# Kernel optimization log

Measured on AMD Instinct MI355X. Metric: run time of the kernel, lower is better.

Reference implementation:

```python
import jax, jax.numpy as jnp
import numpy as np

T, B, OBS, H, A = 512, 256, 128, 256, 32

def setup_inputs() -> dict:
    key = jax.random.key(0)
    ks = jax.random.split(key, 16)
    s = 0.05
    return {
        'hidden': jnp.zeros((B, H), jnp.float32),
        'obs': jax.random.normal(ks[0], (T, B, OBS), jnp.float32),
        'dones': jax.random.bernoulli(ks[1], 0.1, (T, B)),
        'avail_actions': (jax.random.uniform(ks[2], (T, B, A)) > 0.1).astype(jnp.float32),
        'W_emb': jax.random.normal(ks[3], (OBS, H), jnp.float32) * s,
        'b_emb': jnp.zeros((H,), jnp.float32),
        'Wi': jax.random.normal(ks[4], (H, 3 * H), jnp.float32) * s,
        'bi': jnp.zeros((3 * H,), jnp.float32),
        'Whr': jax.random.normal(ks[5], (H, H), jnp.float32) * s,
        'Whz': jax.random.normal(ks[6], (H, H), jnp.float32) * s,
        'Whn': jax.random.normal(ks[7], (H, H), jnp.float32) * s,
        'bhn': jnp.zeros((H,), jnp.float32),
        'W_a1': jax.random.normal(ks[8], (H, H), jnp.float32) * s,
        'b_a1': jnp.zeros((H,), jnp.float32),
        'W_a2': jax.random.normal(ks[9], (H, A), jnp.float32) * s,
        'b_a2': jnp.zeros((A,), jnp.float32),
        'W_c1': jax.random.normal(ks[10], (H, H), jnp.float32) * s,
        'b_c1': jnp.zeros((H,), jnp.float32),
        'W_c2': jax.random.normal(ks[11], (H, 1), jnp.float32) * s,
        'b_c2': jnp.zeros((1,), jnp.float32),
    }

def reference(hidden, obs, dones, avail_actions, W_emb, b_emb, Wi, bi,
              Whr, Whz, Whn, bhn, W_a1, b_a1, W_a2, b_a2, W_c1, b_c1, W_c2, b_c2):
    # obs embedding + relu: [T,B,OBS] -> [T,B,H]
    emb = jax.nn.relu(obs @ W_emb + b_emb)
    # precompute input gate projections for all timesteps (same math as per-step Dense)
    gi = emb @ Wi + bi  # [T,B,3H]

    def step(h, xs):
        gi_t, done_t = xs
        h = jnp.where(done_t[:, None], 0.0, h)  # reset-select to zero init carry
        ir, iz, inn = jnp.split(gi_t, 3, axis=-1)
        r = jax.nn.sigmoid(ir + h @ Whr)
        z = jax.nn.sigmoid(iz + h @ Whz)
        n = jnp.tanh(inn + r * (h @ Whn + bhn))
        h_new = (1.0 - z) * n + z * h
        return h_new, h_new

    hidden_out, y = jax.lax.scan(step, hidden, (gi, dones))  # y: [T,B,H]

    actor_h = jax.nn.relu(y @ W_a1 + b_a1)
    actor_mean = actor_h @ W_a2 + b_a2  # [T,B,A]
    logits = actor_mean - (1.0 - avail_actions) * 1e10

    critic_h = jax.nn.relu(y @ W_c1 + b_c1)
    value = jnp.squeeze(critic_h @ W_c2 + b_c2, axis=-1)  # [T,B]
    return hidden_out, logits, value
```

## Files before the change

### kernel.cpp

```cpp
#include <hip/hip_runtime.h>
#include <stdint.h>

#define T_DIM 512
#define B_DIM 256
#define OBS_DIM 128
#define H_DIM 256
#define A_DIM 32
#define TB (T_DIM*B_DIM)

typedef unsigned short u16;
typedef unsigned int   u32;
typedef _Float16 half2v __attribute__((ext_vector_type(2)));
typedef __attribute__((ext_vector_type(8))) short short8;
typedef __attribute__((ext_vector_type(4))) float f32x4;
typedef __attribute__((ext_vector_type(4))) u32   u32x4;

__device__ __forceinline__ float bf2f(u16 v){ return __uint_as_float(((u32)v)<<16); }
__device__ __forceinline__ u16 f2bf(float f){
    u32 x = __float_as_uint(f);
    u32 r = x + 0x7fffu + ((x>>16)&1u);
    return (u16)(r>>16);
}
__device__ __forceinline__ float2 bfpair(u32 u){
    return make_float2(__uint_as_float(u<<16), __uint_as_float(u & 0xffff0000u));
}

__device__ __forceinline__ float dot2(u32 a, u32 b, float c){
#if __has_builtin(__builtin_amdgcn_fdot2)
    return __builtin_amdgcn_fdot2(__builtin_bit_cast(half2v,a),
                                  __builtin_bit_cast(half2v,b), c, false);
#else
    half2v ha = __builtin_bit_cast(half2v,a), hb = __builtin_bit_cast(half2v,b);
    return fmaf((float)ha[0],(float)hb[0], fmaf((float)ha[1],(float)hb[1], c));
#endif
}

#define DOT2A(acc, w, h) \
    asm("v_dot2_f32_f16 %0, %1, %2, %0" : "+v"(acc) : "v"(w), "v"(h))

#define GLOAD16(gsrc, ldst) \
    __builtin_amdgcn_global_load_lds( \
        (const __attribute__((address_space(1))) void*)(gsrc), \
        (__attribute__((address_space(3))) void*)(ldst), 16, 0, 0)

__global__ void zero_flags_kernel(int* p){ if(threadIdx.x<4) p[threadIdx.x]=0; }

__global__ void detect_kernel(const unsigned char* __restrict__ d, int n, int* __restrict__ flags){
    int f=0;
    for(int p = blockIdx.x*blockDim.x+threadIdx.x; p<n; p += gridDim.x*blockDim.x){
        if(d[p]){ int m=p&3; if(m==1) f|=1; else if(m>=2) f|=2; }
    }
    if(f) atomicOr(flags, f);
}

__global__ void concat_bias_kernel(const float* __restrict__ a, const float* __restrict__ b,
                                   float* __restrict__ dst){
    int i = threadIdx.x;
    dst[i] = a[i];
    dst[256 + i] = b[i];
}

__global__ void cvt_wt_kernel(const float* __restrict__ Whr, const float* __restrict__ Whz,
                              const float* __restrict__ Whn, u32* __restrict__ dst){
    int i = blockIdx.x*blockDim.x + threadIdx.x;
    if(i >= 3*32*256*4) return;
    int e = i & 3;
    int j = (i >> 2) & 255;
    int q = (i >> 10) & 31;
    int m = i >> 15;
    const float* W = (m==0) ? Whr : (m==1) ? Whz : Whn;
    int kp = q*4 + e, k = 2*kp;
    _Float16 lo = (_Float16)W[(size_t)k    *H_DIM + j];
    _Float16 hi = (_Float16)W[(size_t)(k+1)*H_DIM + j];
    dst[i] = (u32)__builtin_bit_cast(u16,lo) | ((u32)__builtin_bit_cast(u16,hi) << 16);
}

__global__ void cvt_wT_kernel(const float* __restrict__ W, u16* __restrict__ dst,
                              int K, int N){
    int i = blockIdx.x*blockDim.x + threadIdx.x;
    if(i >= K*N) return;
    int n = i / K;
    int k = i - n*K;
    dst[i] = f2bf(W[(size_t)k*N + n]);
}

template<int RELU, int AF32>
__global__ __launch_bounds__(256, 2)
void gemm_mfma_kernel(const void* __restrict__ A_, const u16* __restrict__ Bt,
                      const float* __restrict__ bias, u16* __restrict__ C,
                      int M, int N, int K)
{
    __shared__ u16 As[128*32];
    __shared__ u16 Bs[128*32];
    const int tid  = threadIdx.x;
    const int wave = tid >> 6;
    const int lane = tid & 63;
    const int ln15 = lane & 15;
    const int quad = lane >> 4;
    const int wm = wave & 1, wn = wave >> 1;
    const int rowBase = blockIdx.y*128;
    const int colBase = blockIdx.x*128;

    f32x4 acc[4][4] = {};

    const int rA   = tid >> 2;
    const int cA   = (tid & 3) * 8;
    u16* AsW0 = As + wave*512;
    u16* AsW1 = As + 2048 + wave*512;
    u16* BsW0 = Bs + wave*512;
    u16* BsW1 = Bs + 2048 + wave*512;

    const int sr = tid >> 1;
    const int sc = (tid & 1) * 16;

    for(int kb = 0; kb < K; kb += 32){
        if(AF32){
            const float* af = (const float*)A_;
            const float* ag = af + (size_t)(rowBase+sr)*K + kb + sc;
            float4 f0 = *(const float4*)ag;
            float4 f1 = *(const float4*)(ag+4);
            float4 f2 = *(const float4*)(ag+8);
            float4 f3 = *(const float4*)(ag+12);
            u16 tmp[16] = { f2bf(f0.x),f2bf(f0.y),f2bf(f0.z),f2bf(f0.w),
                            f2bf(f1.x),f2bf(f1.y),f2bf(f1.z),f2bf(f1.w),
                            f2bf(f2.x),f2bf(f2.y),f2bf(f2.z),f2bf(f2.w),
                            f2bf(f3.x),f2bf(f3.y),f2bf(f3.z),f2bf(f3.w) };
            *(uint4*)&As[sr*32 + sc]     = *(const uint4*)&tmp[0];
            *(uint4*)&As[sr*32 + sc + 8] = *(const uint4*)&tmp[8];
        } else {
            const u16* ab = (const u16*)A_;
            GLOAD16(ab + (size_t)(rowBase +      rA)*K + kb + cA, AsW0);
            GLOAD16(ab + (size_t)(rowBase + 64 + rA)*K + kb + cA, AsW1);
        }
        GLOAD16(Bt + (size_t)(colBase +      rA)*K + kb + cA, BsW0);
        GLOAD16(Bt + (size_t)(colBase + 64 + rA)*K + kb + cA, BsW1);
        __syncthreads();

        short8 af[4], bf[4];
        #pragma unroll
        for(int mt=0;mt<4;mt++)
            af[mt] = *(const short8*)&As[(wm*64+mt*16+ln15)*32 + quad*8];
        #pragma unroll
        for(int nt=0;nt<4;nt++)
            bf[nt] = *(const short8*)&Bs[(wn*64+nt*16+ln15)*32 + quad*8];
        #pragma unroll
        for(int mt=0;mt<4;mt++){
            #pragma unroll
            for(int nt=0;nt<4;nt++){
                acc[mt][nt] = __builtin_amdgcn_mfma_f32_16x16x32_bf16(
                                  af[mt], bf[nt], acc[mt][nt], 0, 0, 0);
            }
        }
        __syncthreads();
    }

    #pragma unroll
    for(int nt=0;nt<4;nt++){
        int n = colBase + wn*64 + nt*16 + ln15;
        float bv = bias[n];
        #pragma unroll
        for(int mt=0;mt<4;mt++){
            #pragma unroll
            for(int r=0;r<4;r++){
                int m = rowBase + wm*64 + mt*16 + quad*4 + r;
                float v = acc[mt][nt][r] + bv;
                if(RELU) v = fmaxf(v, 0.f);
                C[(size_t)m*N + n] = f2bf(v);
            }
        }
    }
}

__global__ __attribute__((amdgpu_flat_work_group_size(1024,1024), amdgpu_waves_per_eu(4,4)))
void scan_kernel(const u16* __restrict__ gi, const void* __restrict__ dones,
                 const int* __restrict__ flags, const u32x4* __restrict__ Wt4,
                 const float* __restrict__ bhn, float* __restrict__ h_carry,
                 u16* __restrict__ y, int t0, int Tc)
{
    __shared__ __align__(16) u32 hbuf[2][128];
    __shared__ float rex[3][4][256];
    const int tid = threadIdx.x;
    const int j   = tid & 255;
    const int g   = tid >> 8;
    const int row = blockIdx.x;
    const int fl  = flags[0];
    const int mode = (fl&1) ? 0 : ((fl&2) ? 2 : 1);

    auto getdone = [&](int t)->bool{
        int idx = t*B_DIM + row;
        if(mode==0) return ((const unsigned char*)dones)[idx] != 0;
        if(mode==1) return ((const int*)dones)[idx] != 0;
        return ((const float*)dones)[idx] != 0.f;
    };

    const u32x4* baseR = Wt4 + (size_t)( 0 + g*8)*256 + j;
    const u32x4* baseZ = Wt4 + (size_t)(32 + g*8)*256 + j;
    const u32x4* baseN = Wt4 + (size_t)(64 + g*8)*256 + j;
    u32 wr[32], wz[32], wn[32];
    #pragma unroll
    for(int q=0;q<8;q++){
        u32x4 tr = baseR[(size_t)q*256]; wr[4*q]=tr[0]; wr[4*q+1]=tr[1]; wr[4*q+2]=tr[2]; wr[4*q+3]=tr[3];
        u32x4 tz = baseZ[(size_t)q*256]; wz[4*q]=tz[0]; wz[4*q+1]=tz[1]; wz[4*q+2]=tz[2]; wz[4*q+3]=tz[3];
        u32x4 tn = baseN[(size_t)q*256]; wn[4*q]=tn[0]; wn[4*q+1]=tn[1]; wn[4*q+2]=tn[2]; wn[4*q+3]=tn[3];
    }

    const float bh = bhn[j];
    float hoj = 0.f;
    if(g == 0){
        bool d0 = getdone(t0);
        hoj = d0 ? 0.f : h_carry[(size_t)row*H_DIM + j];
        ((_Float16*)hbuf[0])[j] = (_Float16)hoj;
    }
    __syncthreads();

    int cur = 0;
    for(int t=0; t<Tc; ++t){
        size_t gbase = ((size_t)t*B_DIM + row)*768;
        float ir=0.f, izv=0.f, inn=0.f; bool dn=false;
        if(g == 0){
            ir  = bf2f(gi[gbase + j]);
            izv = bf2f(gi[gbase + 256 + j]);
            inn = bf2f(gi[gbase + 512 + j]);
            dn  = (t < Tc-1) ? getdone(t0+t+1) : false;
        }

        float r0=0.f,r1=0.f,z0=0.f,z1=0.f,n0=0.f,n1=0.f;
        const u32x4* hb = (const u32x4*)hbuf[cur] + g*8;
        #pragma unroll
        for(int q=0;q<8;q++){
            u32x4 hv = hb[q];
            DOT2A(r0, wr[4*q  ], hv[0]); DOT2A(r1, wr[4*q+1], hv[1]);
            DOT2A(r0, wr[4*q+2], hv[2]); DOT2A(r1, wr[4*q+3], hv[3]);
            DOT2A(z0, wz[4*q  ], hv[0]); DOT2A(z1, wz[4*q+1], hv[1]);
            DOT2A(z0, wz[4*q+2], hv[2]); DOT2A(z1, wz[4*q+3], hv[3]);
            DOT2A(n0, wn[4*q  ], hv[0]); DOT2A(n1, wn[4*q+1], hv[1]);
            DOT2A(n0, wn[4*q+2], hv[2]); DOT2A(n1, wn[4*q+3], hv[3]);
        }
        if(g != 0){
            rex[0][g][j] = r0 + r1;
            rex[1][g][j] = z0 + z1;
            rex[2][g][j] = n0 + n1;
        }
        __syncthreads();

        if(g == 0){
            float rt = (r0 + r1) + rex[0][1][j] + (rex[0][2][j] + rex[0][3][j]);
            float zt = (z0 + z1) + rex[1][1][j] + (rex[1][2][j] + rex[1][3][j]);
            float nt = (n0 + n1) + rex[2][1][j] + (rex[2][2][j] + rex[2][3][j]);
            float r = 1.f/(1.f + __expf(-(ir + rt)));
            float z = 1.f/(1.f + __expf(-(izv + zt)));
            float x = inn + r*(nt + bh);
            float e2 = __expf(2.f*x);
            float n = 1.f - 2.f/(e2 + 1.f);
            float hn = (1.f - z)*n + z*hoj;
            hoj = dn ? 0.f : hn;
            ((_Float16*)hbuf[cur^1])[j] = (_Float16)hoj;
            y[((size_t)t*B_DIM + row)*H_DIM + j] = f2bf(hn);
        }
        __syncthreads();
        cur ^= 1;
    }

    if(g == 0) h_carry[(size_t)row*H_DIM + j] = hoj;
}

__global__ __launch_bounds__(256)
void heads_kernel(const u16* __restrict__ ac, int ld, const float* __restrict__ W_a2,
                  const float* __restrict__ b_a2, const float* __restrict__ avail,
                  const float* __restrict__ W_c2, const float* __restrict__ b_c2,
                  float* __restrict__ logits, float* __restrict__ value)
{
    __shared__ u16 ahs[64][264];
    const int tid = threadIdx.x;
    const int r0 = blockIdx.x*64;
    {
        int row = tid & 63;
        int c0 = (tid >> 6) * 64;
        const uint4* gp = (const uint4*)(ac + (size_t)(r0+row)*ld + c0);
        #pragma unroll
        for(int q=0;q<8;q++){
            uint4 u = gp[q];
            u32* dst = (u32*)&ahs[row][c0 + q*8];
            dst[0]=u.x; dst[1]=u.y; dst[2]=u.z; dst[3]=u.w;
        }
    }
    __syncthreads();
    const int c  = tid & 31;
    const int rg = tid >> 5;
    float acc[8]={0.f,0.f,0.f,0.f,0.f,0.f,0.f,0.f};
    float bc = b_a2[c];
    for(int k=0;k<H_DIM;k+=4){
        float w0 = W_a2[(k+0)*A_DIM + c];
        float w1 = W_a2[(k+1)*A_DIM + c];
        float w2 = W_a2[(k+2)*A_DIM + c];
        float w3 = W_a2[(k+3)*A_DIM + c];
        #pragma unroll
        for(int rr=0;rr<8;rr++){
            uint2 av = *(const uint2*)&ahs[rg*8+rr][k];
            float2 p0 = bfpair(av.x), p1 = bfpair(av.y);
            acc[rr] = fmaf(p0.x,w0,fmaf(p0.y,w1,fmaf(p1.x,w2,fmaf(p1.y,w3,acc[rr]))));
        }
    }
    #pragma unroll
    for(int rr=0;rr<8;rr++){
        int grow = r0 + rg*8 + rr;
        float av = avail[(size_t)grow*A_DIM + c];
        logits[(size_t)grow*A_DIM + c] = acc[rr] + bc - (1.f-av)*1e10f;
    }

    const int lane = tid & 63;
    const int wid  = tid >> 6;
    const u16* ch  = ac + 256;
    float4 wv = *(const float4*)(W_c2 + lane*4);
    float bcv = b_c2[0];
    uint2 cv[16];
    #pragma unroll
    for(int i=0;i<16;i++){
        int row = r0 + wid*16 + i;
        cv[i] = *(const uint2*)(ch + (size_t)row*ld + lane*4);
    }
    #pragma unroll
    for(int i=0;i<16;i++){
        float2 p0 = bfpair(cv[i].x), p1 = bfpair(cv[i].y);
        float a2 = p0.x*wv.x + p0.y*wv.y + p1.x*wv.z + p1.y*wv.w;
        #pragma unroll
        for(int off=32; off>0; off>>=1) a2 += __shfl_down(a2, off, 64);
        if(lane==0) value[r0 + wid*16 + i] = a2 + bcv;
    }
}

extern "C" void kernel_launch(void* const* d_in, const int* in_sizes, int n_in,
                              void* d_out, int out_size, void* d_ws, size_t ws_size,
                              hipStream_t stream)
{
    const float* hidden = (const float*)d_in[0];
    const float* obs    = (const float*)d_in[1];
    const void*  dones  = d_in[2];
    const float* avail  = (const float*)d_in[3];
    const float* W_emb  = (const float*)d_in[4];
    const float* b_emb  = (const float*)d_in[5];
    const float* Wi     = (const float*)d_in[6];
    const float* bi     = (const float*)d_in[7];
    const float* Whr    = (const float*)d_in[8];
    const float* Whz    = (const float*)d_in[9];
    const float* Whn    = (const float*)d_in[10];
    const float* bhn    = (const float*)d_in[11];
    const float* W_a1   = (const float*)d_in[12];
    const float* b_a1   = (const float*)d_in[13];
    const float* W_a2   = (const float*)d_in[14];
    const float* b_a2   = (const float*)d_in[15];
    const float* W_c1   = (const float*)d_in[16];
    const float* b_c1   = (const float*)d_in[17];
    const float* W_c2   = (const float*)d_in[18];
    const float* b_c2   = (const float*)d_in[19];

    float* out_hidden = (float*)d_out;
    float* out_logits = out_hidden + (size_t)B_DIM*H_DIM;
    float* out_value  = out_logits + (size_t)TB*A_DIM;

    const size_t fixed = 393216 + 393216 + 262144 + 65536 + 262144 + 256 + 2048;
    int Tc = 4;
    for(int cand = 256; cand >= 4; cand >>= 1){
        size_t need = fixed + (size_t)cand*(393216  + 262144  + 131072 );
        if(need <= ws_size){ Tc = cand; break; }
    }
    const int NC = T_DIM / Tc;

    uint8_t* ws = (uint8_t*)d_ws;
    size_t off = 0;
    u32*  wt_b    = (u32*)(ws + off); off += 393216;
    u16*  wiT     = (u16*)(ws + off); off += 393216;
    u16*  wacT    = (u16*)(ws + off); off += 262144;
    u16*  wembT   = (u16*)(ws + off); off += 65536;
    float* h_carry= (float*)(ws + off); off += 262144;
    int*  flags   = (int*)(ws + off); off += 256;
    float* b_ac   = (float*)(ws + off); off += 2048;
    u16*  gi_c    = (u16*)(ws + off); off += (size_t)Tc*393216;
    u16*  embac_c = (u16*)(ws + off); off += (size_t)Tc*262144;
    u16*  y_c     = (u16*)(ws + off); off += (size_t)Tc*131072;
    u16*  emb_c   = embac_c;
    u16*  ac_c    = embac_c;

    zero_flags_kernel<<<1, 64, 0, stream>>>(flags);
    detect_kernel<<<64, 256, 0, stream>>>((const unsigned char*)dones, TB, flags);
    cvt_wt_kernel<<<384, 256, 0, stream>>>(Whr, Whz, Whn, wt_b);
    cvt_wT_kernel<<<768, 256, 0, stream>>>(Wi,   wiT,  256, 768);
    cvt_wT_kernel<<<256, 256, 0, stream>>>(W_a1, wacT,          256, 256);
    cvt_wT_kernel<<<256, 256, 0, stream>>>(W_c1, wacT + 65536,  256, 256);
    cvt_wT_kernel<<<128, 256, 0, stream>>>(W_emb, wembT, 128, 256);
    concat_bias_kernel<<<1, 256, 0, stream>>>(b_a1, b_c1, b_ac);
    hipMemcpyAsync(h_carry, hidden, (size_t)B_DIM*H_DIM*sizeof(float),
                   hipMemcpyDeviceToDevice, stream);

    const int Mc = Tc*B_DIM;
    const int gy = Mc/128;

    for(int c = 0; c < NC; ++c){
        const int t0 = c*Tc;
        const float* obs_c = obs + (size_t)t0*B_DIM*OBS_DIM;
        gemm_mfma_kernel<1,1><<<dim3(2,gy), 256, 0, stream>>>(obs_c, wembT, b_emb, emb_c, Mc, 256, 128);
        gemm_mfma_kernel<0,0><<<dim3(6,gy), 256, 0, stream>>>(emb_c, wiT, bi, gi_c, Mc, 768, 256);
        scan_kernel<<<256, 1024, 0, stream>>>(gi_c, dones, flags, (const u32x4*)wt_b,
                                              bhn, h_carry, y_c, t0, Tc);
        gemm_mfma_kernel<1,0><<<dim3(4,gy), 256, 0, stream>>>(y_c, wacT, b_ac, ac_c, Mc, 512, 256);
        heads_kernel<<<Mc/64, 256, 0, stream>>>(ac_c, 512, W_a2, b_a2,
                                                avail + (size_t)t0*B_DIM*A_DIM,
                                                W_c2, b_c2,
                                                out_logits + (size_t)t0*B_DIM*A_DIM,
                                                out_value + (size_t)t0*B_DIM);
    }

    hipMemcpyAsync(out_hidden, h_carry, (size_t)B_DIM*H_DIM*sizeof(float),
                   hipMemcpyDeviceToDevice, stream);
}
```

Measured before the change: 1.133 ms.

## Split GRU scan K-reduction within each wave and reduce with shuffles

Reassigns threads so that each wave owns 16 hidden columns and its four 16-lane quarters split the K dimension, instead of four 256-thread groups splitting K across waves. The partial dot products are combined with xor-shuffles inside the wave, which removes the shared-memory exchange buffer and one block-wide barrier per timestep. In exchange, the gate math and the global loads/stores now run on only 16 of every 64 lanes spread over all 16 waves, so per-wave divergence rises and the y/gi accesses are split into 16-element segments per wave.

```diff
diff --git a/kernel.cpp b/kernel.cpp
--- a/kernel.cpp
+++ b/kernel.cpp
@@ -178,12 +178,13 @@
                  u16* __restrict__ y, int t0, int Tc)
 {
     __shared__ __align__(16) u32 hbuf[2][128];
-    __shared__ float rex[3][4][256];
-    const int tid = threadIdx.x;
-    const int j   = tid & 255;
-    const int g   = tid >> 8;
-    const int row = blockIdx.x;
-    const int fl  = flags[0];
+    const int tid  = threadIdx.x;
+    const int wave = tid >> 6;
+    const int lane = tid & 63;
+    const int col  = wave*16 + (lane & 15);
+    const int qd   = lane >> 4;
+    const int row  = blockIdx.x;
+    const int fl   = flags[0];
     const int mode = (fl&1) ? 0 : ((fl&2) ? 2 : 1);
 
     auto getdone = [&](int t)->bool{
@@ -193,9 +194,9 @@
         return ((const float*)dones)[idx] != 0.f;
     };
 
-    const u32x4* baseR = Wt4 + (size_t)( 0 + g*8)*256 + j;
-    const u32x4* baseZ = Wt4 + (size_t)(32 + g*8)*256 + j;
-    const u32x4* baseN = Wt4 + (size_t)(64 + g*8)*256 + j;
+    const u32x4* baseR = Wt4 + (size_t)( 0 + qd*8)*256 + col;
+    const u32x4* baseZ = Wt4 + (size_t)(32 + qd*8)*256 + col;
+    const u32x4* baseN = Wt4 + (size_t)(64 + qd*8)*256 + col;
     u32 wr[32], wz[32], wn[32];
     #pragma unroll
     for(int q=0;q<8;q++){
@@ -204,12 +205,12 @@
         u32x4 tn = baseN[(size_t)q*256]; wn[4*q]=tn[0]; wn[4*q+1]=tn[1]; wn[4*q+2]=tn[2]; wn[4*q+3]=tn[3];
     }
 
-    const float bh = bhn[j];
+    const float bh = bhn[col];
     float hoj = 0.f;
-    if(g == 0){
+    if(lane < 16){
         bool d0 = getdone(t0);
-        hoj = d0 ? 0.f : h_carry[(size_t)row*H_DIM + j];
-        ((_Float16*)hbuf[0])[j] = (_Float16)hoj;
+        hoj = d0 ? 0.f : h_carry[(size_t)row*H_DIM + col];
+        ((_Float16*)hbuf[0])[col] = (_Float16)hoj;
     }
     __syncthreads();
 
@@ -217,15 +218,15 @@
     for(int t=0; t<Tc; ++t){
         size_t gbase = ((size_t)t*B_DIM + row)*768;
         float ir=0.f, izv=0.f, inn=0.f; bool dn=false;
-        if(g == 0){
-            ir  = bf2f(gi[gbase + j]);
-            izv = bf2f(gi[gbase + 256 + j]);
-            inn = bf2f(gi[gbase + 512 + j]);
+        if(lane < 16){
+            ir  = bf2f(gi[gbase + col]);
+            izv = bf2f(gi[gbase + 256 + col]);
+            inn = bf2f(gi[gbase + 512 + col]);
             dn  = (t < Tc-1) ? getdone(t0+t+1) : false;
         }
 
         float r0=0.f,r1=0.f,z0=0.f,z1=0.f,n0=0.f,n1=0.f;
-        const u32x4* hb = (const u32x4*)hbuf[cur] + g*8;
+        const u32x4* hb = (const u32x4*)hbuf[cur] + qd*8;
         #pragma unroll
         for(int q=0;q<8;q++){
             u32x4 hv = hb[q];
@@ -236,32 +237,28 @@
             DOT2A(n0, wn[4*q  ], hv[0]); DOT2A(n1, wn[4*q+1], hv[1]);
             DOT2A(n0, wn[4*q+2], hv[2]); DOT2A(n1, wn[4*q+3], hv[3]);
         }
-        if(g != 0){
-            rex[0][g][j] = r0 + r1;
-            rex[1][g][j] = z0 + z1;
-            rex[2][g][j] = n0 + n1;
-        }
-        __syncthreads();
-
-        if(g == 0){
-            float rt = (r0 + r1) + rex[0][1][j] + (rex[0][2][j] + rex[0][3][j]);
-            float zt = (z0 + z1) + rex[1][1][j] + (rex[1][2][j] + rex[1][3][j]);
-            float nt = (n0 + n1) + rex[2][1][j] + (rex[2][2][j] + rex[2][3][j]);
-            float r = 1.f/(1.f + __expf(-(ir + rt)));
-            float z = 1.f/(1.f + __expf(-(izv + zt)));
-            float x = inn + r*(nt + bh);
+
+        float rs = r0 + r1, zs = z0 + z1, ns = n0 + n1;
+        rs += __shfl_xor(rs, 16, 64);  rs += __shfl_xor(rs, 32, 64);
+        zs += __shfl_xor(zs, 16, 64);  zs += __shfl_xor(zs, 32, 64);
+        ns += __shfl_xor(ns, 16, 64);  ns += __shfl_xor(ns, 32, 64);
+
+        if(lane < 16){
+            float r = 1.f/(1.f + __expf(-(ir + rs)));
+            float z = 1.f/(1.f + __expf(-(izv + zs)));
+            float x = inn + r*(ns + bh);
             float e2 = __expf(2.f*x);
             float n = 1.f - 2.f/(e2 + 1.f);
             float hn = (1.f - z)*n + z*hoj;
             hoj = dn ? 0.f : hn;
-            ((_Float16*)hbuf[cur^1])[j] = (_Float16)hoj;
-            y[((size_t)t*B_DIM + row)*H_DIM + j] = f2bf(hn);
+            ((_Float16*)hbuf[cur^1])[col] = (_Float16)hoj;
+            y[((size_t)t*B_DIM + row)*H_DIM + col] = f2bf(hn);
         }
         __syncthreads();
         cur ^= 1;
     }
 
-    if(g == 0) h_carry[(size_t)row*H_DIM + j] = hoj;
+    if(lane < 16) h_carry[(size_t)row*H_DIM + col] = hoj;
 }
 
 __global__ __launch_bounds__(256)
```

After: 1.435 ms. +26.6%, slower.
